# Kernel tuning notes

Hardware: AMD Instinct MI355X
Metric: run time of the kernel (lower is better)

The kernel has to match this reference:

```python
import jax, jax.numpy as jnp
import numpy as np

B, C, H, W = 4, 128, 256, 256
KMAX = 29  # kernel_size_max; all per-channel sizes are odd and <= KMAX


def _ragged_mask():
    # jagged odd kernel sizes growing with distance (channel index): 5..29
    ksizes = np.linspace(5, KMAX, C).astype(np.int64)
    ksizes = ksizes - (1 - ksizes % 2)  # force odd parity (matches 'same' centering)
    mask = np.zeros((C, 1, KMAX, KMAX), dtype=np.float32)
    for i, k in enumerate(ksizes):
        s = (KMAX - k) // 2  # start_idx = (kmax - k)//2 as in configure()
        mask[i, 0, s:s + k, s:s + k] = 1.0
    return jnp.asarray(mask)


def setup_inputs() -> dict:
    key = jax.random.key(0)
    kx, kk = jax.random.split(key)
    x = jax.random.normal(kx, (B, C, H, W), dtype=jnp.float32)
    kernels = jax.random.normal(kk, (C, 1, KMAX, KMAX), dtype=jnp.float32) * 0.05
    kernels = kernels * _ragged_mask()  # zero outside each channel's k_i x k_i window
    return {"x": x, "kernels": kernels}


def reference(x, kernels):
    # Per-channel conv with varying kernel size, expressed as a single fused
    # depthwise conv: each ragged kernel is centered in a zero-padded KMAX window,
    # which with 'same' padding and matching odd parity is exactly equivalent to
    # the original split -> per-channel Conv2d(k_i, padding='same') -> concat.
    c = x.shape[1]
    return jax.lax.conv_general_dilated(
        x, kernels,
        window_strides=(1, 1),
        padding='SAME',
        feature_group_count=c,
        dimension_numbers=('NCHW', 'OIHW', 'NCHW'))
```

## Files before the change

kernel.cpp:

```cpp
#include <hip/hip_runtime.h>


#define C_CH    128
#define HW      256
#define KMAX    29
#define TILE_W  128
#define TILE_H  64
#define ROWH    184
#define ROWU    92
#define STAGE_W 88
#define MAXR    92

typedef __fp16 f16x8 __attribute__((ext_vector_type(8)));
typedef float  f32x4 __attribute__((ext_vector_type(4)));
typedef __fp16 half2_t __attribute__((ext_vector_type(2)));

__device__ __forceinline__ unsigned pack_f16(float a, float b) {
    half2_t h = __builtin_amdgcn_cvt_pkrtz(a, b);
    union { half2_t h; unsigned u; } cvt; cvt.h = h; return cvt.u;
}
__device__ __forceinline__ f16x8 uint4_as_f16x8(uint4 v) {
    union { uint4 u; f16x8 h; } cvt; cvt.u = v; return cvt.h;
}
__device__ __forceinline__ half2_t u32_as_h2(unsigned u) {
    union { unsigned u; half2_t h; } cvt; cvt.u = u; return cvt.h;
}
__device__ __forceinline__ int ragged_k(int c) {
    int kk = (int)(5.0 + 24.0 * (double)c / 127.0);
    kk -= (1 - (kk & 1));
    return kk;
}

__global__ __launch_bounds__(128)
void prepack_frags(const float* __restrict__ kern, uint4* __restrict__ wf)
{
    const int c   = blockIdx.x;
    const int dy  = blockIdx.y;
    const int tid = threadIdx.x;
    const int strip = tid >> 6;
    const int lane  = tid & 63;
    const int kk = ragged_k(c);
    const int s  = (KMAX - kk) >> 1;
    const int n  = lane & 15;
    const int kb = lane >> 4;
    const float* wrow = kern + c * (KMAX * KMAX) + dy * KMAX;
    unsigned u[4];
    #pragma unroll
    for (int r = 0; r < 4; ++r) {
        float v[2];
        #pragma unroll
        for (int h = 0; h < 2; ++h) {
            const int k = strip * 32 + kb * 8 + 2 * r + h;
            const int d = k - n;
            v[h] = (d >= 0 && d < kk) ? wrow[d + s] : 0.0f;
        }
        u[r] = pack_f16(v[0], v[1]);
    }
    wf[(size_t)((c * KMAX + dy) * 2 + strip) * 64 + lane] =
        make_uint4(u[0], u[1], u[2], u[3]);
}

__global__ __launch_bounds__(256, 4)
void jagged_conv_mfma(const float* __restrict__ x,
                      const uint4* __restrict__ wf,
                      float* __restrict__ out)
{
    const int bx = blockIdx.x;
    const int by = blockIdx.y;
    const int bc = blockIdx.z;
    const int c  = bc & (C_CH - 1);
    const int kk = ragged_k(c);
    const int s  = (KMAX - kk) >> 1;
    const int R  = TILE_H + kk - 1;

    __shared__ __align__(16) unsigned tile[MAXR * ROWU];

    const int tid = threadIdx.x;
    const int rbase = by * TILE_H + s - 14;
    const int cbase = bx * TILE_W + s - 14;
    const float* xin = x + (size_t)bc * (HW * HW);

    for (int i = tid; i < R * STAGE_W; i += 256) {
        const int r = i / STAGE_W;
        const int p = i - r * STAGE_W;
        const int gy = rbase + r;
        const int gx = cbase + 2 * p;
        float a = 0.0f, b = 0.0f;
        if ((unsigned)gy < HW) {
            const float* row = xin + gy * HW;
            if ((unsigned)gx < HW)       a = row[gx];
            if ((unsigned)(gx + 1) < HW) b = row[gx + 1];
        }
        tile[r * ROWU + p] = pack_f16(a, b);
    }
    __syncthreads();

    const int lane = tid & 63;
    const int w    = tid >> 6;
    const int ml   = lane & 15;
    const int kb   = lane >> 4;

    f32x4 a0 = {0,0,0,0}, a1 = {0,0,0,0}, a2 = {0,0,0,0}, a3 = {0,0,0,0};
    f32x4 a4 = {0,0,0,0}, a5 = {0,0,0,0}, a6 = {0,0,0,0}, a7 = {0,0,0,0};

    const __fp16* hp = (const __fp16*)tile;
    const __fp16* ap = hp + (16 * w + ml) * ROWH + 8 * kb;
    const uint4* wp = wf + (size_t)c * (KMAX * 2 * 64) + (size_t)(2 * s) * 64 + lane;

    const bool two = (kk > 17);

    uint4 nb0 = wp[0];
    uint4 nb1 = two ? wp[64] : nb0;

    for (int d = 0; d < kk; ++d) {
        const uint4 b0 = nb0;
        const uint4 b1 = nb1;
        wp += 128;
        if (d + 1 < kk) {
            nb0 = wp[0];
            if (two) nb1 = wp[64];
        }

        f16x8 F0 = *(const f16x8*)(ap +   0);
        f16x8 F1 = *(const f16x8*)(ap +  16);
        f16x8 F2 = *(const f16x8*)(ap +  32);
        f16x8 F3 = *(const f16x8*)(ap +  48);
        f16x8 F4 = *(const f16x8*)(ap +  64);
        f16x8 F5 = *(const f16x8*)(ap +  80);
        f16x8 F6 = *(const f16x8*)(ap +  96);
        f16x8 F7 = *(const f16x8*)(ap + 112);

        f16x8 B0 = uint4_as_f16x8(b0);
        a0 = __builtin_amdgcn_mfma_f32_16x16x32_f16(F0, B0, a0, 0, 0, 0);
        a1 = __builtin_amdgcn_mfma_f32_16x16x32_f16(F1, B0, a1, 0, 0, 0);
        a2 = __builtin_amdgcn_mfma_f32_16x16x32_f16(F2, B0, a2, 0, 0, 0);
        a3 = __builtin_amdgcn_mfma_f32_16x16x32_f16(F3, B0, a3, 0, 0, 0);
        a4 = __builtin_amdgcn_mfma_f32_16x16x32_f16(F4, B0, a4, 0, 0, 0);
        a5 = __builtin_amdgcn_mfma_f32_16x16x32_f16(F5, B0, a5, 0, 0, 0);
        a6 = __builtin_amdgcn_mfma_f32_16x16x32_f16(F6, B0, a6, 0, 0, 0);
        a7 = __builtin_amdgcn_mfma_f32_16x16x32_f16(F7, B0, a7, 0, 0, 0);

        if (two) {
            f16x8 F8 = *(const f16x8*)(ap + 128);
            f16x8 F9 = *(const f16x8*)(ap + 144);
            f16x8 B1 = uint4_as_f16x8(b1);
            a0 = __builtin_amdgcn_mfma_f32_16x16x32_f16(F2, B1, a0, 0, 0, 0);
            a1 = __builtin_amdgcn_mfma_f32_16x16x32_f16(F3, B1, a1, 0, 0, 0);
            a2 = __builtin_amdgcn_mfma_f32_16x16x32_f16(F4, B1, a2, 0, 0, 0);
            a3 = __builtin_amdgcn_mfma_f32_16x16x32_f16(F5, B1, a3, 0, 0, 0);
            a4 = __builtin_amdgcn_mfma_f32_16x16x32_f16(F6, B1, a4, 0, 0, 0);
            a5 = __builtin_amdgcn_mfma_f32_16x16x32_f16(F7, B1, a5, 0, 0, 0);
            a6 = __builtin_amdgcn_mfma_f32_16x16x32_f16(F8, B1, a6, 0, 0, 0);
            a7 = __builtin_amdgcn_mfma_f32_16x16x32_f16(F9, B1, a7, 0, 0, 0);
        }
        ap += ROWH;
    }

    float* op = out + (size_t)bc * (HW * HW)
              + (size_t)(by * TILE_H + 16 * w + 4 * kb) * HW
              + bx * TILE_W + ml;
    #pragma unroll
    for (int r = 0; r < 4; ++r) {
        op[r * HW +   0] = a0[r];
        op[r * HW +  16] = a1[r];
        op[r * HW +  32] = a2[r];
        op[r * HW +  48] = a3[r];
        op[r * HW +  64] = a4[r];
        op[r * HW +  80] = a5[r];
        op[r * HW +  96] = a6[r];
        op[r * HW + 112] = a7[r];
    }
}

#define FB_TILE 64
#define PAD     14
#define LDS_R   92
#define ROW_U32 52

__global__ __launch_bounds__(512)
void prepack_weights(const float* __restrict__ kern, unsigned* __restrict__ wp)
{
    const int c = blockIdx.x;
    const int tid = threadIdx.x;
    if (tid >= 29 * 16) return;
    const int dy = tid >> 4;
    const int t  = tid & 15;
    float w0 = 0.0f, w1 = 0.0f;
    if (2 * t < KMAX)     w0 = kern[c * (KMAX * KMAX) + dy * KMAX + 2 * t];
    if (2 * t + 1 < KMAX) w1 = kern[c * (KMAX * KMAX) + dy * KMAX + 2 * t + 1];
    wp[(c * KMAX + dy) * 16 + t] = pack_f16(w0, w1);
}

__global__ __launch_bounds__(256, 4)
void jagged_conv_kernel(const float* __restrict__ x,
                        const unsigned* __restrict__ wp,
                        float* __restrict__ out)
{
    const int bx = blockIdx.x;
    const int by = blockIdx.y;
    const int bc = blockIdx.z;
    const int c  = bc & (C_CH - 1);

    int kk = ragged_k(c);
    const int s  = (KMAX - kk) >> 1;
    const int t0 = s >> 1;
    const int t1 = (s + kk - 1) >> 1;

    __shared__ __align__(16) unsigned tile[LDS_R * ROW_U32];

    const int tid = threadIdx.x;
    const int gy0 = by * FB_TILE - PAD;
    const int gx0 = bx * FB_TILE - PAD;
    const float* xin = x + (size_t)bc * (HW * HW);

    for (int i = tid; i < LDS_R * ROW_U32; i += 256) {
        const int r = i / ROW_U32;
        const int p = i - r * ROW_U32;
        const int gy = gy0 + r;
        const int gx = gx0 + 2 * p;
        float a = 0.0f, b = 0.0f;
        if ((unsigned)gy < HW) {
            const float* row = xin + gy * HW;
            if ((unsigned)gx < HW)       a = row[gx];
            if ((unsigned)(gx + 1) < HW) b = row[gx + 1];
        }
        tile[i] = pack_f16(a, b);
    }
    __syncthreads();

    const int tx = tid & 7;
    const int ty = tid >> 3;

    float acc[2][8];
    #pragma unroll
    for (int j = 0; j < 2; ++j)
        #pragma unroll
        for (int p = 0; p < 8; ++p) acc[j][p] = 0.0f;

    const unsigned* wch = wp + c * (KMAX * 16);

    const int rend = s + kk + 1;
    for (int rr = s; rr < rend; ++rr) {
        const uint4* lp = (const uint4*)&tile[(ty * 2 + rr) * ROW_U32 + tx * 4];
        unsigned seg[20];
        {
            uint4 v0 = lp[0], v1 = lp[1], v2 = lp[2], v3 = lp[3], v4 = lp[4];
            seg[0]=v0.x; seg[1]=v0.y; seg[2]=v0.z; seg[3]=v0.w;
            seg[4]=v1.x; seg[5]=v1.y; seg[6]=v1.z; seg[7]=v1.w;
            seg[8]=v2.x; seg[9]=v2.y; seg[10]=v2.z; seg[11]=v2.w;
            seg[12]=v3.x; seg[13]=v3.y; seg[14]=v3.z; seg[15]=v3.w;
            seg[16]=v4.x; seg[17]=v4.y; seg[18]=v4.z; seg[19]=v4.w;
        }
        unsigned sseg[18];
        #pragma unroll
        for (int k = 0; k < 18; ++k)
            sseg[k] = __builtin_amdgcn_alignbit(seg[k + 1], seg[k], 16);

        #pragma unroll
        for (int j = 0; j < 2; ++j) {
            const int dy = rr - j;
            if (dy >= s && dy < s + kk) {
                const unsigned* wrow = wch + dy * 16;
                unsigned wv[16];
                #pragma unroll
                for (int t = 0; t < 16; ++t) wv[t] = wrow[t];
                #pragma unroll
                for (int t = 0; t < 15; ++t) {
                    if (t >= t0 && t <= t1) {
                        const half2_t wh = u32_as_h2(wv[t]);
                        acc[j][0] = __builtin_amdgcn_fdot2(u32_as_h2(seg[t + 0]), wh, acc[j][0], false);
                        acc[j][2] = __builtin_amdgcn_fdot2(u32_as_h2(seg[t + 1]), wh, acc[j][2], false);
                        acc[j][4] = __builtin_amdgcn_fdot2(u32_as_h2(seg[t + 2]), wh, acc[j][4], false);
                        acc[j][6] = __builtin_amdgcn_fdot2(u32_as_h2(seg[t + 3]), wh, acc[j][6], false);
                        acc[j][1] = __builtin_amdgcn_fdot2(u32_as_h2(sseg[t + 0]), wh, acc[j][1], false);
                        acc[j][3] = __builtin_amdgcn_fdot2(u32_as_h2(sseg[t + 1]), wh, acc[j][3], false);
                        acc[j][5] = __builtin_amdgcn_fdot2(u32_as_h2(sseg[t + 2]), wh, acc[j][5], false);
                        acc[j][7] = __builtin_amdgcn_fdot2(u32_as_h2(sseg[t + 3]), wh, acc[j][7], false);
                    }
                }
            }
        }
    }

    float* op = out + (size_t)bc * (HW * HW);
    const int ox = bx * FB_TILE + tx * 8;
    #pragma unroll
    for (int j = 0; j < 2; ++j) {
        const int oy = by * FB_TILE + ty * 2 + j;
        float4 o0 = make_float4(acc[j][0], acc[j][1], acc[j][2], acc[j][3]);
        float4 o1 = make_float4(acc[j][4], acc[j][5], acc[j][6], acc[j][7]);
        *(float4*)(op + (size_t)oy * HW + ox)     = o0;
        *(float4*)(op + (size_t)oy * HW + ox + 4) = o1;
    }
}

extern "C" void kernel_launch(void* const* d_in, const int* in_sizes, int n_in,
                              void* d_out, int out_size, void* d_ws, size_t ws_size,
                              hipStream_t stream) {
    const float* x    = (const float*)d_in[0];
    const float* kern = (const float*)d_in[1];
    float* out        = (float*)d_out;

    const size_t WF_BYTES = (size_t)C_CH * KMAX * 2 * 64 * 16;

    if (ws_size >= WF_BYTES) {
        uint4* wf = (uint4*)d_ws;
        prepack_frags<<<dim3(C_CH, KMAX), dim3(128), 0, stream>>>(kern, wf);
        dim3 grid(HW / TILE_W, HW / TILE_H, 4 * C_CH);
        jagged_conv_mfma<<<grid, dim3(256), 0, stream>>>(x, wf, out);
    } else {
        unsigned* wpack = (unsigned*)d_ws;
        prepack_weights<<<dim3(C_CH), dim3(512), 0, stream>>>(kern, wpack);
        dim3 grid(HW / FB_TILE, HW / FB_TILE, 4 * C_CH);
        jagged_conv_kernel<<<grid, dim3(256), 0, stream>>>(x, wpack, out);
    }
}
```

Measured before the change: 324.2 us.

## Vectorize input staging with aligned float4 loads and remap block order

Input staging now has each wave handle whole rows, with lanes issuing aligned float4 global loads and uint2 LDS stores, replacing scalar pairwise loads. This relies on shifting the tile origin by an alignment offset e and folding that offset into the prepacked weight fragments. The block index is also remapped so that co-resident blocks cover grouped channel/spatial tiles, which is meant to improve L2 locality. The change aims to cut global load instruction count and uncoalesced access, at the cost of extra index arithmetic and a tight coupling between the alignment offset and the weight layout.

New measurement: 306.7 us. 5.4% less time.

```diff
diff --git a/kernel.cpp b/kernel.cpp
--- a/kernel.cpp
+++ b/kernel.cpp
@@ -8,8 +8,8 @@
 #define TILE_H  64
 #define ROWH    184
 #define ROWU    92
-#define STAGE_W 88
 #define MAXR    92
+#define WQ      44
 
 typedef __fp16 f16x8 __attribute__((ext_vector_type(8)));
 typedef float  f32x4 __attribute__((ext_vector_type(4)));
@@ -41,6 +41,7 @@
     const int lane  = tid & 63;
     const int kk = ragged_k(c);
     const int s  = (KMAX - kk) >> 1;
+    const int e  = (s + 2) & 7;
     const int n  = lane & 15;
     const int kb = lane >> 4;
     const float* wrow = kern + c * (KMAX * KMAX) + dy * KMAX;
@@ -51,7 +52,7 @@
         #pragma unroll
         for (int h = 0; h < 2; ++h) {
             const int k = strip * 32 + kb * 8 + 2 * r + h;
-            const int d = k - n;
+            const int d = k - n - e;
             v[h] = (d >= 0 && d < kk) ? wrow[d + s] : 0.0f;
         }
         u[r] = pack_f16(v[0], v[1]);
@@ -65,40 +66,55 @@
                       const uint4* __restrict__ wf,
                       float* __restrict__ out)
 {
-    const int bx = blockIdx.x;
-    const int by = blockIdx.y;
-    const int bc = blockIdx.z;
+    const int L  = blockIdx.x + 2 * (blockIdx.y + 4 * blockIdx.z);
+    const int X  = L & 7;
+    const int g  = L >> 3;
+    const int bc = X * 64 + (g >> 3);
+    const int sp = g & 7;
+    const int bx = sp & 1;
+    const int by = sp >> 1;
+
     const int c  = bc & (C_CH - 1);
     const int kk = ragged_k(c);
     const int s  = (KMAX - kk) >> 1;
+    const int e  = (s + 2) & 7;
     const int R  = TILE_H + kk - 1;
 
     __shared__ __align__(16) unsigned tile[MAXR * ROWU];
 
-    const int tid = threadIdx.x;
-    const int rbase = by * TILE_H + s - 14;
-    const int cbase = bx * TILE_W + s - 14;
-    const float* xin = x + (size_t)bc * (HW * HW);
-
-    for (int i = tid; i < R * STAGE_W; i += 256) {
-        const int r = i / STAGE_W;
-        const int p = i - r * STAGE_W;
-        const int gy = rbase + r;
-        const int gx = cbase + 2 * p;
-        float a = 0.0f, b = 0.0f;
-        if ((unsigned)gy < HW) {
-            const float* row = xin + gy * HW;
-            if ((unsigned)gx < HW)       a = row[gx];
-            if ((unsigned)(gx + 1) < HW) b = row[gx + 1];
-        }
-        tile[r * ROWU + p] = pack_f16(a, b);
-    }
-    __syncthreads();
-
+    const int tid  = threadIdx.x;
     const int lane = tid & 63;
     const int w    = tid >> 6;
-    const int ml   = lane & 15;
-    const int kb   = lane >> 4;
+    const int rbase  = by * TILE_H + s - 14;
+    const int galign = bx * TILE_W + s - 14 - e;
+    const float* xin = x + (size_t)bc * (HW * HW);
+
+    for (int r = w; r < R; r += 4) {
+        const int gy = rbase + r;
+        if (lane < WQ) {
+            unsigned lo = 0, hi = 0;
+            if ((unsigned)gy < HW) {
+                const int gx = galign + 4 * lane;
+                const float* row = xin + gy * HW;
+                float4 v;
+                if ((unsigned)gx <= (HW - 4)) {
+                    v = *(const float4*)(row + gx);
+                } else {
+                    v.x = ((unsigned)(gx + 0) < HW) ? row[gx + 0] : 0.0f;
+                    v.y = ((unsigned)(gx + 1) < HW) ? row[gx + 1] : 0.0f;
+                    v.z = ((unsigned)(gx + 2) < HW) ? row[gx + 2] : 0.0f;
+                    v.w = ((unsigned)(gx + 3) < HW) ? row[gx + 3] : 0.0f;
+                }
+                lo = pack_f16(v.x, v.y);
+                hi = pack_f16(v.z, v.w);
+            }
+            *(uint2*)&tile[r * ROWU + 2 * lane] = make_uint2(lo, hi);
+        }
+    }
+    __syncthreads();
+
+    const int ml = lane & 15;
+    const int kb = lane >> 4;
 
     f32x4 a0 = {0,0,0,0}, a1 = {0,0,0,0}, a2 = {0,0,0,0}, a3 = {0,0,0,0};
     f32x4 a4 = {0,0,0,0}, a5 = {0,0,0,0}, a6 = {0,0,0,0}, a7 = {0,0,0,0};
```
